# Kernel tuning notes

Measured on AMD Instinct MI355X. Metric: run time of the kernel, lower is better.

## Reference

```python
import jax, jax.numpy as jnp
import numpy as np

V, D, C, NUM_CLASSES = 50000, 128, 128, 200
N, S = 4096, 128
NUM_VIDEOS = 256
KSIZES = (3, 4, 5)


def setup_inputs() -> dict:
    key = jax.random.key(0)
    ks = jax.random.split(key, 10)
    input_x = jax.random.randint(ks[0], (N, 1, S), 0, V)
    # sorted segment ids, every video non-empty (contiguous ragged segments)
    segment_ids = ((jnp.arange(N) * NUM_VIDEOS) // N).astype(jnp.int32)
    emb = jax.random.normal(ks[1], (V, D), dtype=jnp.float32) * (2.0 / (V + D)) ** 0.5  # xavier_normal
    W3 = jax.random.normal(ks[2], (3, D, C), dtype=jnp.float32) * 0.05
    b3 = jnp.zeros((C,), dtype=jnp.float32)
    W4 = jax.random.normal(ks[3], (4, D, C), dtype=jnp.float32) * 0.05
    b4 = jnp.zeros((C,), dtype=jnp.float32)
    W5 = jax.random.normal(ks[4], (5, D, C), dtype=jnp.float32) * 0.05
    b5 = jnp.zeros((C,), dtype=jnp.float32)
    Wout = jax.random.normal(ks[5], (3 * C, NUM_CLASSES), dtype=jnp.float32) * 0.05
    bout = jnp.zeros((NUM_CLASSES,), dtype=jnp.float32)
    return {"input_x": input_x, "segment_ids": segment_ids, "emb": emb,
            "W3": W3, "b3": b3, "W4": W4, "b4": b4, "W5": W5, "b5": b5,
            "Wout": Wout, "bout": bout}


def _conv_maxpool(x, W, b):
    # x: [N, S, D], W: [w, D, C] -> conv over time (VALID), then max over time -> [N, C]
    y = jax.lax.conv_general_dilated(x, W, window_strides=(1,), padding='VALID',
                                     dimension_numbers=('NWC', 'WIO', 'NWC')) + b
    return jnp.max(y, axis=1)


def reference(input_x, segment_ids, emb, W3, b3, W4, b4, W5, b5, Wout, bout):
    x = emb[input_x[:, 0, :]]                       # [N, S, D]
    feat = jnp.concatenate([_conv_maxpool(x, W3, b3),
                            _conv_maxpool(x, W4, b4),
                            _conv_maxpool(x, W5, b5)], axis=1)  # [N, 3C]
    logits = feat @ Wout + bout                     # [N, num_classes]
    scores = jax.nn.sigmoid(logits)
    # ragged per-video max over contiguous text rows
    video_scores = jax.ops.segment_max(scores, segment_ids, num_segments=NUM_VIDEOS)
    return video_scores
```

## Files before the change

kernel.cpp:

```cpp
#include <hip/hip_runtime.h>
#include <hip/hip_bf16.h>


using bf16_t  = __bf16;
using bf16x4  = __attribute__((ext_vector_type(4))) __bf16;
using bf16x8  = __attribute__((ext_vector_type(8))) __bf16;
using floatx4 = __attribute__((ext_vector_type(4))) float;

#define N_SENT 4096
#define S_LEN  128
#define D_DIM  128
#define C_DIM  128
#define NCLS   200
#define NVID   256
#define V_SZ   50000

#define X_ROWS   132
#define X_STRIDE 136

#define BP3_OFF 0
#define BP4_OFF 49152
#define BP5_OFF 114688
#define BPACK_ELEMS 196608

#define FEAT_OFF  (1u << 20)
#define EMB16_OFF (8u << 20)

__global__ void prep_emb(const float* __restrict__ emb, bf16_t* __restrict__ emb16) {
  int i4 = blockIdx.x * 256 + threadIdx.x;
  const floatx4 f = __builtin_nontemporal_load((const floatx4*)emb + i4);
  bf16x4 h;
  h.x = (bf16_t)f.x; h.y = (bf16_t)f.y; h.z = (bf16_t)f.z; h.w = (bf16_t)f.w;
  __builtin_nontemporal_store(h, (bf16x4*)emb16 + i4);
}

__global__ void prep_bpack(const float* __restrict__ W3,
                           const float* __restrict__ W4,
                           const float* __restrict__ W5,
                           bf16_t* __restrict__ bpack) {
  int idx = blockIdx.x * 256 + threadIdx.x;
  if (idx >= BPACK_ELEMS) return;
  int KS; const float* W; int rel;
  if (idx < BP4_OFF)      { KS = 3; W = W3; rel = idx; }
  else if (idx < BP5_OFF) { KS = 4; W = W4; rel = idx - BP4_OFF; }
  else                    { KS = 5; W = W5; rel = idx - BP5_OFF; }
  int szct  = 2048 * KS;
  int ctile = rel / szct;
  int r2    = rel - ctile * szct;
  int g     = r2 >> 7;
  int r3    = r2 & 127;
  int n     = r3 >> 3;
  int j     = r3 & 7;
  bpack[idx] = (bf16_t)W[(g * 8 + j) * C_DIM + (ctile * 16 + n)];
}

template <int KS>
__device__ __forceinline__ void conv_k(const bf16_t* Ab,
                                       const bf16_t* bp0, const bf16_t* bp1,
                                       const bf16_t* bp2, const bf16_t* bp3,
                                       float* __restrict__ pms,
                                       int m, int q, int lane, int rbase) {
  floatx4 acc[4][4];
#pragma unroll
  for (int ct = 0; ct < 4; ++ct)
#pragma unroll
    for (int mt = 0; mt < 4; ++mt)
      acc[ct][mt] = (floatx4){0.f, 0.f, 0.f, 0.f};

#pragma unroll 1
  for (int c0 = 0; c0 < KS; ++c0) {
    bf16x8 B0[4], B1[4], B2[4], B3[4];
#pragma unroll
    for (int st = 0; st < 4; ++st) {
      B0[st] = *(const bf16x8*)(bp0 + st * 512);
      B1[st] = *(const bf16x8*)(bp1 + st * 512);
      B2[st] = *(const bf16x8*)(bp2 + st * 512);
      B3[st] = *(const bf16x8*)(bp3 + st * 512);
    }
    bp0 += 2048; bp1 += 2048; bp2 += 2048; bp3 += 2048;
#pragma unroll
    for (int mt = 0; mt < 4; ++mt) {
#pragma unroll
      for (int st = 0; st < 4; ++st) {
        const bf16x8 a = *(const bf16x8*)(Ab + mt * 16 * X_STRIDE + st * 32);
        acc[0][mt] = __builtin_amdgcn_mfma_f32_16x16x32_bf16(a, B0[st], acc[0][mt], 0, 0, 0);
        acc[1][mt] = __builtin_amdgcn_mfma_f32_16x16x32_bf16(a, B1[st], acc[1][mt], 0, 0, 0);
        acc[2][mt] = __builtin_amdgcn_mfma_f32_16x16x32_bf16(a, B2[st], acc[2][mt], 0, 0, 0);
        acc[3][mt] = __builtin_amdgcn_mfma_f32_16x16x32_bf16(a, B3[st], acc[3][mt], 0, 0, 0);
      }
    }
    Ab += X_STRIDE;
  }

  const int tlim = S_LEN - KS + 1;
#pragma unroll
  for (int ct = 0; ct < 4; ++ct) {
    float mx = -__builtin_inff();
#pragma unroll
    for (int mt = 0; mt < 4; ++mt)
#pragma unroll
      for (int r = 0; r < 4; ++r) {
        const int t = rbase + mt * 16 + q * 4 + r;
        if (t < tlim) mx = fmaxf(mx, acc[ct][mt][r]);
      }
    mx = fmaxf(mx, __shfl_xor(mx, 16));
    mx = fmaxf(mx, __shfl_xor(mx, 32));
    if (lane < 16) pms[ct * 16 + m] = mx;
  }
}

__global__ __launch_bounds__(256, 3) void conv_gemm(
    const int* __restrict__ input_x, const bf16_t* __restrict__ emb16,
    const bf16_t* __restrict__ bpack, const float* __restrict__ b3,
    const float* __restrict__ b4, const float* __restrict__ b5,
    float* __restrict__ feat) {
  __shared__ __align__(16) bf16_t Xs[X_ROWS * X_STRIDE];
  __shared__ float pm[3 * 2 * 128];
  const int sent = blockIdx.x;
  const int tid  = threadIdx.x;

  {
    const int rip = tid >> 4;
    const int l16 = tid & 15;
#pragma unroll
    for (int r0 = 0; r0 < S_LEN; r0 += 16) {
      const int row   = r0 + rip;
      const int token = __builtin_nontemporal_load(&input_x[sent * S_LEN + row]);
      const bf16x8 v  =
          __builtin_nontemporal_load((const bf16x8*)(emb16 + token * D_DIM + l16 * 8));
      *(bf16x8*)(&Xs[row * X_STRIDE + l16 * 8]) = v;
    }
    for (int i = tid; i < 4 * X_STRIDE; i += 256)
      Xs[128 * X_STRIDE + i] = (bf16_t)0.f;
  }
  __syncthreads();

  const int wv   = tid >> 6;
  const int lane = tid & 63;
  const int m    = lane & 15;
  const int q    = lane >> 4;
  const int mh   = wv >> 1;
  const int ch   = wv & 1;
  const bf16_t* Ab = Xs + (mh * 64 + m) * X_STRIDE + q * 8;
  const int blaneoff = q * 128 + m * 8;
  const int cb   = ch * 4;

  conv_k<3>(Ab, bpack + BP3_OFF + (cb + 0) * 6144 + blaneoff,
                bpack + BP3_OFF + (cb + 1) * 6144 + blaneoff,
                bpack + BP3_OFF + (cb + 2) * 6144 + blaneoff,
                bpack + BP3_OFF + (cb + 3) * 6144 + blaneoff,
            &pm[(0 * 2 + mh) * 128 + ch * 64], m, q, lane, mh * 64);
  __builtin_amdgcn_sched_barrier(0);
  conv_k<4>(Ab, bpack + BP4_OFF + (cb + 0) * 8192 + blaneoff,
                bpack + BP4_OFF + (cb + 1) * 8192 + blaneoff,
                bpack + BP4_OFF + (cb + 2) * 8192 + blaneoff,
                bpack + BP4_OFF + (cb + 3) * 8192 + blaneoff,
            &pm[(1 * 2 + mh) * 128 + ch * 64], m, q, lane, mh * 64);
  __builtin_amdgcn_sched_barrier(0);
  conv_k<5>(Ab, bpack + BP5_OFF + (cb + 0) * 10240 + blaneoff,
                bpack + BP5_OFF + (cb + 1) * 10240 + blaneoff,
                bpack + BP5_OFF + (cb + 2) * 10240 + blaneoff,
                bpack + BP5_OFF + (cb + 3) * 10240 + blaneoff,
            &pm[(2 * 2 + mh) * 128 + ch * 64], m, q, lane, mh * 64);

  __syncthreads();

  for (int i = tid; i < 384; i += 256) {
    const int sec = i >> 7;
    const int c   = i & 127;
    const float v = fmaxf(pm[(sec * 2 + 0) * 128 + c],
                          pm[(sec * 2 + 1) * 128 + c]);
    const float* bs = (sec == 0) ? b3 : ((sec == 1) ? b4 : b5);
    __builtin_nontemporal_store(v + bs[c], &feat[sent * 384 + i]);
  }
}

__global__ void classify(const float* __restrict__ feat,
                         const float* __restrict__ Wout,
                         const float* __restrict__ bout,
                         float* __restrict__ out) {
  __shared__ float fs[16 * 384];
  const int vid = blockIdx.x;
  const int tid = threadIdx.x;
  for (int i = tid; i < 16 * 384; i += 256) fs[i] = feat[vid * 16 * 384 + i];
  __syncthreads();
  if (tid < NCLS) {
    float acc[16];
#pragma unroll
    for (int s = 0; s < 16; ++s) acc[s] = 0.f;
    for (int d = 0; d < 384; ++d) {
      const float wv = Wout[d * NCLS + tid];
#pragma unroll
      for (int s = 0; s < 16; ++s) acc[s] = fmaf(fs[s * 384 + d], wv, acc[s]);
    }
    const float b = bout[tid];
    float vmax = -__builtin_inff();
#pragma unroll
    for (int s = 0; s < 16; ++s) {
      const float sc = 1.f / (1.f + __expf(-(acc[s] + b)));
      vmax = fmaxf(vmax, sc);
    }
    out[vid * NCLS + tid] = vmax;
  }
}

extern "C" void kernel_launch(void* const* d_in, const int* in_sizes, int n_in,
                              void* d_out, int out_size, void* d_ws, size_t ws_size,
                              hipStream_t stream) {
  const int*   input_x = (const int*)d_in[0];
  const float* emb  = (const float*)d_in[2];
  const float* W3   = (const float*)d_in[3];
  const float* b3   = (const float*)d_in[4];
  const float* W4   = (const float*)d_in[5];
  const float* b4   = (const float*)d_in[6];
  const float* W5   = (const float*)d_in[7];
  const float* b5   = (const float*)d_in[8];
  const float* Wout = (const float*)d_in[9];
  const float* bout = (const float*)d_in[10];

  bf16_t* bpack = (bf16_t*)d_ws;
  float*  feat  = (float*)((char*)d_ws + FEAT_OFF);
  bf16_t* emb16 = (bf16_t*)((char*)d_ws + EMB16_OFF);
  float*  out   = (float*)d_out;

  prep_emb<<<(V_SZ * D_DIM) / 4 / 256, 256, 0, stream>>>(emb, emb16);
  prep_bpack<<<BPACK_ELEMS / 256, 256, 0, stream>>>(W3, W4, W5, bpack);
  conv_gemm<<<N_SENT, 256, 0, stream>>>(input_x, emb16, bpack, b3, b4, b5, feat);
  classify<<<NVID, 256, 0, stream>>>(feat, Wout, bout, out);
}
```

Measured before the change: 301.5 us.

## Process two sentences per block, stream B per k-step, rotate conv order

Each conv_gemm block now handles two sentences with 512 threads, and launch bounds change to (512,4). The inner loop loads B fragments per k-step instead of holding all 16 in registers, which lowers register pressure. The loop is wrapped in s_setprio around the MFMA bursts. Waves also rotate the order of the 3/4/5 kernel sizes so concurrent waves touch different weight sections and avoid contending on the same loads. In exchange, LDS use per block doubles and B loads sit closer to the MFMAs, so load latency may be exposed.

```diff
diff --git a/kernel.cpp b/kernel.cpp
--- a/kernel.cpp
+++ b/kernel.cpp
@@ -69,26 +69,24 @@
 
 #pragma unroll 1
   for (int c0 = 0; c0 < KS; ++c0) {
-    bf16x8 B0[4], B1[4], B2[4], B3[4];
 #pragma unroll
     for (int st = 0; st < 4; ++st) {
-      B0[st] = *(const bf16x8*)(bp0 + st * 512);
-      B1[st] = *(const bf16x8*)(bp1 + st * 512);
-      B2[st] = *(const bf16x8*)(bp2 + st * 512);
-      B3[st] = *(const bf16x8*)(bp3 + st * 512);
+      const bf16x8 B0 = *(const bf16x8*)(bp0 + st * 512);
+      const bf16x8 B1 = *(const bf16x8*)(bp1 + st * 512);
+      const bf16x8 B2 = *(const bf16x8*)(bp2 + st * 512);
+      const bf16x8 B3 = *(const bf16x8*)(bp3 + st * 512);
+      __builtin_amdgcn_s_setprio(1);
+#pragma unroll
+      for (int mt = 0; mt < 4; ++mt) {
+        const bf16x8 a = *(const bf16x8*)(Ab + mt * 16 * X_STRIDE + st * 32);
+        acc[0][mt] = __builtin_amdgcn_mfma_f32_16x16x32_bf16(a, B0, acc[0][mt], 0, 0, 0);
+        acc[1][mt] = __builtin_amdgcn_mfma_f32_16x16x32_bf16(a, B1, acc[1][mt], 0, 0, 0);
+        acc[2][mt] = __builtin_amdgcn_mfma_f32_16x16x32_bf16(a, B2, acc[2][mt], 0, 0, 0);
+        acc[3][mt] = __builtin_amdgcn_mfma_f32_16x16x32_bf16(a, B3, acc[3][mt], 0, 0, 0);
+      }
+      __builtin_amdgcn_s_setprio(0);
     }
     bp0 += 2048; bp1 += 2048; bp2 += 2048; bp3 += 2048;
-#pragma unroll
-    for (int mt = 0; mt < 4; ++mt) {
-#pragma unroll
-      for (int st = 0; st < 4; ++st) {
-        const bf16x8 a = *(const bf16x8*)(Ab + mt * 16 * X_STRIDE + st * 32);
-        acc[0][mt] = __builtin_amdgcn_mfma_f32_16x16x32_bf16(a, B0[st], acc[0][mt], 0, 0, 0);
-        acc[1][mt] = __builtin_amdgcn_mfma_f32_16x16x32_bf16(a, B1[st], acc[1][mt], 0, 0, 0);
-        acc[2][mt] = __builtin_amdgcn_mfma_f32_16x16x32_bf16(a, B2[st], acc[2][mt], 0, 0, 0);
-        acc[3][mt] = __builtin_amdgcn_mfma_f32_16x16x32_bf16(a, B3[st], acc[3][mt], 0, 0, 0);
-      }
-    }
     Ab += X_STRIDE;
   }
 
@@ -109,29 +107,34 @@
   }
 }
 
-__global__ __launch_bounds__(256, 3) void conv_gemm(
+__global__ __launch_bounds__(512, 4) void conv_gemm(
     const int* __restrict__ input_x, const bf16_t* __restrict__ emb16,
     const bf16_t* __restrict__ bpack, const float* __restrict__ b3,
     const float* __restrict__ b4, const float* __restrict__ b5,
     float* __restrict__ feat) {
-  __shared__ __align__(16) bf16_t Xs[X_ROWS * X_STRIDE];
-  __shared__ float pm[3 * 2 * 128];
-  const int sent = blockIdx.x;
-  const int tid  = threadIdx.x;
+  __shared__ __align__(16) bf16_t Xs[2 * X_ROWS * X_STRIDE];
+  __shared__ float pm[2 * 3 * 2 * 128];
+  const int sent0 = blockIdx.x * 2;
+  const int tid   = threadIdx.x;
 
   {
     const int rip = tid >> 4;
     const int l16 = tid & 15;
 #pragma unroll
-    for (int r0 = 0; r0 < S_LEN; r0 += 16) {
-      const int row   = r0 + rip;
-      const int token = __builtin_nontemporal_load(&input_x[sent * S_LEN + row]);
+    for (int r0 = 0; r0 < 2 * S_LEN; r0 += 32) {
+      const int row = r0 + rip;
+      const int s   = row >> 7;
+      const int r   = row & 127;
+      const int token = __builtin_nontemporal_load(&input_x[(sent0 + s) * S_LEN + r]);
       const bf16x8 v  =
           __builtin_nontemporal_load((const bf16x8*)(emb16 + token * D_DIM + l16 * 8));
-      *(bf16x8*)(&Xs[row * X_STRIDE + l16 * 8]) = v;
-    }
-    for (int i = tid; i < 4 * X_STRIDE; i += 256)
-      Xs[128 * X_STRIDE + i] = (bf16_t)0.f;
+      *(bf16x8*)(&Xs[(s * X_ROWS + r) * X_STRIDE + l16 * 8]) = v;
+    }
+    for (int i = tid; i < 2 * 4 * X_STRIDE; i += 512) {
+      const int s = (i >= 4 * X_STRIDE);
+      const int o = i - s * (4 * X_STRIDE);
+      Xs[(s * X_ROWS + 128) * X_STRIDE + o] = (bf16_t)0.f;
+    }
   }
   __syncthreads();
 
@@ -139,39 +142,52 @@
   const int lane = tid & 63;
   const int m    = lane & 15;
   const int q    = lane >> 4;
-  const int mh   = wv >> 1;
+  const int s    = wv >> 2;
+  const int mh   = (wv >> 1) & 1;
   const int ch   = wv & 1;
-  const bf16_t* Ab = Xs + (mh * 64 + m) * X_STRIDE + q * 8;
+  const bf16_t* Ab = Xs + (s * X_ROWS + mh * 64 + m) * X_STRIDE + q * 8;
   const int blaneoff = q * 128 + m * 8;
   const int cb   = ch * 4;
-
-  conv_k<3>(Ab, bpack + BP3_OFF + (cb + 0) * 6144 + blaneoff,
-                bpack + BP3_OFF + (cb + 1) * 6144 + blaneoff,
-                bpack + BP3_OFF + (cb + 2) * 6144 + blaneoff,
-                bpack + BP3_OFF + (cb + 3) * 6144 + blaneoff,
-            &pm[(0 * 2 + mh) * 128 + ch * 64], m, q, lane, mh * 64);
-  __builtin_amdgcn_sched_barrier(0);
-  conv_k<4>(Ab, bpack + BP4_OFF + (cb + 0) * 8192 + blaneoff,
-                bpack + BP4_OFF + (cb + 1) * 8192 + blaneoff,
-                bpack + BP4_OFF + (cb + 2) * 8192 + blaneoff,
-                bpack + BP4_OFF + (cb + 3) * 8192 + blaneoff,
-            &pm[(1 * 2 + mh) * 128 + ch * 64], m, q, lane, mh * 64);
-  __builtin_amdgcn_sched_barrier(0);
-  conv_k<5>(Ab, bpack + BP5_OFF + (cb + 0) * 10240 + blaneoff,
-                bpack + BP5_OFF + (cb + 1) * 10240 + blaneoff,
-                bpack + BP5_OFF + (cb + 2) * 10240 + blaneoff,
-                bpack + BP5_OFF + (cb + 3) * 10240 + blaneoff,
-            &pm[(2 * 2 + mh) * 128 + ch * 64], m, q, lane, mh * 64);
+  float* pmw = &pm[s * 768];
+
+  const int rot = wv % 3;
+
+#pragma unroll 1
+  for (int i = 0; i < 3; ++i) {
+    int sec = i + rot; if (sec >= 3) sec -= 3;
+    float* pms = &pmw[(sec * 2 + mh) * 128 + ch * 64];
+    if (sec == 0)
+      conv_k<3>(Ab, bpack + BP3_OFF + (cb + 0) * 6144 + blaneoff,
+                    bpack + BP3_OFF + (cb + 1) * 6144 + blaneoff,
+                    bpack + BP3_OFF + (cb + 2) * 6144 + blaneoff,
+                    bpack + BP3_OFF + (cb + 3) * 6144 + blaneoff,
+                pms, m, q, lane, mh * 64);
+    else if (sec == 1)
+      conv_k<4>(Ab, bpack + BP4_OFF + (cb + 0) * 8192 + blaneoff,
+                    bpack + BP4_OFF + (cb + 1) * 8192 + blaneoff,
+                    bpack + BP4_OFF + (cb + 2) * 8192 + blaneoff,
+                    bpack + BP4_OFF + (cb + 3) * 8192 + blaneoff,
+                pms, m, q, lane, mh * 64);
+    else
+      conv_k<5>(Ab, bpack + BP5_OFF + (cb + 0) * 10240 + blaneoff,
+                    bpack + BP5_OFF + (cb + 1) * 10240 + blaneoff,
+                    bpack + BP5_OFF + (cb + 2) * 10240 + blaneoff,
+                    bpack + BP5_OFF + (cb + 3) * 10240 + blaneoff,
+                pms, m, q, lane, mh * 64);
+    __builtin_amdgcn_sched_barrier(0);
+  }
 
   __syncthreads();
 
-  for (int i = tid; i < 384; i += 256) {
-    const int sec = i >> 7;
-    const int c   = i & 127;
-    const float v = fmaxf(pm[(sec * 2 + 0) * 128 + c],
-                          pm[(sec * 2 + 1) * 128 + c]);
+  for (int i = tid; i < 768; i += 512) {
+    const int ss  = i >> 9 ? 1 : (i >= 384);
+    const int j   = i - ss * 384;
+    const int sec = j >> 7;
+    const int c   = j & 127;
+    const float v = fmaxf(pm[ss * 768 + (sec * 2 + 0) * 128 + c],
+                          pm[ss * 768 + (sec * 2 + 1) * 128 + c]);
     const float* bs = (sec == 0) ? b3 : ((sec == 1) ? b4 : b5);
-    __builtin_nontemporal_store(v + bs[c], &feat[sent * 384 + i]);
+    __builtin_nontemporal_store(v + bs[c], &feat[(sent0 + ss) * 384 + j]);
   }
 }
 
@@ -225,6 +241,6 @@
 
   prep_emb<<<(V_SZ * D_DIM) / 4 / 256, 256, 0, stream>>>(emb, emb16);
   prep_bpack<<<BPACK_ELEMS / 256, 256, 0, stream>>>(W3, W4, W5, bpack);
-  conv_gemm<<<N_SENT, 256, 0, stream>>>(input_x, emb16, bpack, b3, b4, b5, feat);
+  conv_gemm<<<N_SENT / 2, 512, 0, stream>>>(input_x, emb16, bpack, b3, b4, b5, feat);
   classify<<<NVID, 256, 0, stream>>>(feat, Wout, bout, out);
 }
```

After: 296.8 us. No clear change (-1.6%).

## Software-pipeline conv MFMA loop and rotate kernel-size order across waves

Applied to the files above, without the earlier changes.

Replaces the per-tap loop that loaded all sixteen B fragments and issued LDS A loads inline with a flattened loop over tap and K-step pairs. The loop prefetches the next B and A fragments one step ahead, so global and LDS latency can overlap the current step's MFMAs. MFMA issue is wrapped in s_setprio. Each wave also starts with a different filter size (3, 4 or 5), which spreads weight-fetch traffic across waves. The prefetch reads one row past the previous padding, so the shared buffer gains an extra zeroed row. The runtime dispatch over kernel size adds code size and may raise register pressure.

```diff
diff --git a/kernel.cpp b/kernel.cpp
--- a/kernel.cpp
+++ b/kernel.cpp
@@ -15,7 +15,7 @@
 #define NVID   256
 #define V_SZ   50000
 
-#define X_ROWS   132
+#define X_ROWS   133
 #define X_STRIDE 136
 
 #define BP3_OFF 0
@@ -67,29 +67,42 @@
     for (int mt = 0; mt < 4; ++mt)
       acc[ct][mt] = (floatx4){0.f, 0.f, 0.f, 0.f};
 
-#pragma unroll 1
-  for (int c0 = 0; c0 < KS; ++c0) {
-    bf16x8 B0[4], B1[4], B2[4], B3[4];
-#pragma unroll
-    for (int st = 0; st < 4; ++st) {
-      B0[st] = *(const bf16x8*)(bp0 + st * 512);
-      B1[st] = *(const bf16x8*)(bp1 + st * 512);
-      B2[st] = *(const bf16x8*)(bp2 + st * 512);
-      B3[st] = *(const bf16x8*)(bp3 + st * 512);
-    }
-    bp0 += 2048; bp1 += 2048; bp2 += 2048; bp3 += 2048;
+  const int NT = 4 * KS;
+
+  bf16x8 Bc0 = *(const bf16x8*)bp0;  bp0 += 512;
+  bf16x8 Bc1 = *(const bf16x8*)bp1;  bp1 += 512;
+  bf16x8 Bc2 = *(const bf16x8*)bp2;  bp2 += 512;
+  bf16x8 Bc3 = *(const bf16x8*)bp3;  bp3 += 512;
+  bf16x8 Ac[4];
+#pragma unroll
+  for (int mt = 0; mt < 4; ++mt)
+    Ac[mt] = *(const bf16x8*)(Ab + mt * 16 * X_STRIDE);
+
+#pragma unroll 2
+  for (int u = 0; u < NT; ++u) {
+    const bf16x8 Bn0 = *(const bf16x8*)bp0;  bp0 += 512;
+    const bf16x8 Bn1 = *(const bf16x8*)bp1;  bp1 += 512;
+    const bf16x8 Bn2 = *(const bf16x8*)bp2;  bp2 += 512;
+    const bf16x8 Bn3 = *(const bf16x8*)bp3;  bp3 += 512;
+    const bf16_t* An = Ab + ((u + 1) >> 2) * X_STRIDE + ((u + 1) & 3) * 32;
+    bf16x8 Anx[4];
+#pragma unroll
+    for (int mt = 0; mt < 4; ++mt)
+      Anx[mt] = *(const bf16x8*)(An + mt * 16 * X_STRIDE);
+
+    __builtin_amdgcn_s_setprio(1);
 #pragma unroll
     for (int mt = 0; mt < 4; ++mt) {
-#pragma unroll
-      for (int st = 0; st < 4; ++st) {
-        const bf16x8 a = *(const bf16x8*)(Ab + mt * 16 * X_STRIDE + st * 32);
-        acc[0][mt] = __builtin_amdgcn_mfma_f32_16x16x32_bf16(a, B0[st], acc[0][mt], 0, 0, 0);
-        acc[1][mt] = __builtin_amdgcn_mfma_f32_16x16x32_bf16(a, B1[st], acc[1][mt], 0, 0, 0);
-        acc[2][mt] = __builtin_amdgcn_mfma_f32_16x16x32_bf16(a, B2[st], acc[2][mt], 0, 0, 0);
-        acc[3][mt] = __builtin_amdgcn_mfma_f32_16x16x32_bf16(a, B3[st], acc[3][mt], 0, 0, 0);
-      }
-    }
-    Ab += X_STRIDE;
+      acc[0][mt] = __builtin_amdgcn_mfma_f32_16x16x32_bf16(Ac[mt], Bc0, acc[0][mt], 0, 0, 0);
+      acc[1][mt] = __builtin_amdgcn_mfma_f32_16x16x32_bf16(Ac[mt], Bc1, acc[1][mt], 0, 0, 0);
+      acc[2][mt] = __builtin_amdgcn_mfma_f32_16x16x32_bf16(Ac[mt], Bc2, acc[2][mt], 0, 0, 0);
+      acc[3][mt] = __builtin_amdgcn_mfma_f32_16x16x32_bf16(Ac[mt], Bc3, acc[3][mt], 0, 0, 0);
+    }
+    __builtin_amdgcn_s_setprio(0);
+
+    Bc0 = Bn0; Bc1 = Bn1; Bc2 = Bn2; Bc3 = Bn3;
+#pragma unroll
+    for (int mt = 0; mt < 4; ++mt) Ac[mt] = Anx[mt];
   }
 
   const int tlim = S_LEN - KS + 1;
@@ -130,7 +143,7 @@
           __builtin_nontemporal_load((const bf16x8*)(emb16 + token * D_DIM + l16 * 8));
       *(bf16x8*)(&Xs[row * X_STRIDE + l16 * 8]) = v;
     }
-    for (int i = tid; i < 4 * X_STRIDE; i += 256)
+    for (int i = tid; i < 5 * X_STRIDE; i += 256)
       Xs[128 * X_STRIDE + i] = (bf16_t)0.f;
   }
   __syncthreads();
@@ -145,23 +158,32 @@
   const int blaneoff = q * 128 + m * 8;
   const int cb   = ch * 4;
 
-  conv_k<3>(Ab, bpack + BP3_OFF + (cb + 0) * 6144 + blaneoff,
-                bpack + BP3_OFF + (cb + 1) * 6144 + blaneoff,
-                bpack + BP3_OFF + (cb + 2) * 6144 + blaneoff,
-                bpack + BP3_OFF + (cb + 3) * 6144 + blaneoff,
-            &pm[(0 * 2 + mh) * 128 + ch * 64], m, q, lane, mh * 64);
-  __builtin_amdgcn_sched_barrier(0);
-  conv_k<4>(Ab, bpack + BP4_OFF + (cb + 0) * 8192 + blaneoff,
-                bpack + BP4_OFF + (cb + 1) * 8192 + blaneoff,
-                bpack + BP4_OFF + (cb + 2) * 8192 + blaneoff,
-                bpack + BP4_OFF + (cb + 3) * 8192 + blaneoff,
-            &pm[(1 * 2 + mh) * 128 + ch * 64], m, q, lane, mh * 64);
-  __builtin_amdgcn_sched_barrier(0);
-  conv_k<5>(Ab, bpack + BP5_OFF + (cb + 0) * 10240 + blaneoff,
-                bpack + BP5_OFF + (cb + 1) * 10240 + blaneoff,
-                bpack + BP5_OFF + (cb + 2) * 10240 + blaneoff,
-                bpack + BP5_OFF + (cb + 3) * 10240 + blaneoff,
-            &pm[(2 * 2 + mh) * 128 + ch * 64], m, q, lane, mh * 64);
+  const int rot = (wv + ((blockIdx.x & 1) << 1)) % 3;
+
+#pragma unroll 1
+  for (int i = 0; i < 3; ++i) {
+    int sec = i + rot; if (sec >= 3) sec -= 3;
+    float* pms = &pm[(sec * 2 + mh) * 128 + ch * 64];
+    if (sec == 0)
+      conv_k<3>(Ab, bpack + BP3_OFF + (cb + 0) * 6144 + blaneoff,
+                    bpack + BP3_OFF + (cb + 1) * 6144 + blaneoff,
+                    bpack + BP3_OFF + (cb + 2) * 6144 + blaneoff,
+                    bpack + BP3_OFF + (cb + 3) * 6144 + blaneoff,
+                pms, m, q, lane, mh * 64);
+    else if (sec == 1)
+      conv_k<4>(Ab, bpack + BP4_OFF + (cb + 0) * 8192 + blaneoff,
+                    bpack + BP4_OFF + (cb + 1) * 8192 + blaneoff,
+                    bpack + BP4_OFF + (cb + 2) * 8192 + blaneoff,
+                    bpack + BP4_OFF + (cb + 3) * 8192 + blaneoff,
+                pms, m, q, lane, mh * 64);
+    else
+      conv_k<5>(Ab, bpack + BP5_OFF + (cb + 0) * 10240 + blaneoff,
+                    bpack + BP5_OFF + (cb + 1) * 10240 + blaneoff,
+                    bpack + BP5_OFF + (cb + 2) * 10240 + blaneoff,
+                    bpack + BP5_OFF + (cb + 3) * 10240 + blaneoff,
+                pms, m, q, lane, mh * 64);
+    __builtin_amdgcn_sched_barrier(0);
+  }
 
   __syncthreads();
 
```

Result: slower. 312.5 us (+3.6%).
